# Kernel optimization log

Measured on AMD Instinct MI355X. Metric: run time of the kernel, lower is better.

The kernel has to match this reference:

```python
import jax, jax.numpy as jnp
import numpy as np

EMB = 128
HEADS = 8
B = 8
T = 2048


def setup_inputs() -> dict:
    key = jax.random.key(0)
    ks = jax.random.split(key, 6)
    x = jax.random.normal(ks[0], (B, T, EMB), dtype=jnp.float32)
    # torch Linear(emb, heads*emb, bias=False): store as (in, out) so y = x @ W
    scale = 1.0 / np.sqrt(EMB)
    Wq = jax.random.uniform(ks[1], (EMB, HEADS * EMB), jnp.float32, -scale, scale)
    Wk = jax.random.uniform(ks[2], (EMB, HEADS * EMB), jnp.float32, -scale, scale)
    Wv = jax.random.uniform(ks[3], (EMB, HEADS * EMB), jnp.float32, -scale, scale)
    so = 1.0 / np.sqrt(HEADS * EMB)
    Wo = jax.random.uniform(ks[4], (HEADS * EMB, EMB), jnp.float32, -so, so)
    bo = jax.random.uniform(ks[5], (EMB,), jnp.float32, -so, so)
    return {"x": x, "Wq": Wq, "Wk": Wk, "Wv": Wv, "Wo": Wo, "bo": bo}


def reference(x, Wq, Wk, Wv, Wo, bo):
    b, t, e = x.shape
    h = HEADS
    q = (x @ Wq).reshape(b, t, h, e)  # [b,t,h,e]
    k = (x @ Wk).reshape(b, t, h, e)
    v = (x @ Wv).reshape(b, t, h, e)
    # scores: [b,h,q,k], scaled by sqrt(e) (per-head dim == emb here)
    scores = jnp.einsum('bqhe,bkhe->bhqk', q, k) / jnp.sqrt(jnp.asarray(e, x.dtype))
    attn = jax.nn.softmax(scores, axis=-1)
    out = jnp.einsum('bhqk,bkhe->bqhe', attn, v).reshape(b, t, h * e)
    return out @ Wo + bo
```

## Files before the change

### kernel.cpp

```cpp
#include <hip/hip_runtime.h>

using bf16x8 = __attribute__((ext_vector_type(8))) short;
using f32x4  = __attribute__((ext_vector_type(4))) float;

__device__ __forceinline__ ushort f2bf(float f) {
    union { float f; unsigned int u; } c; c.f = f;
    unsigned int u = c.u;
    u = (u + 0x7fffu + ((u >> 16) & 1u)) >> 16;
    return (ushort)u;
}

#if defined(__has_builtin)
#if __has_builtin(__builtin_amdgcn_cvt_pk_bf16_f32)
#define HAS_PK_BF16 1
#endif
#endif
__device__ __forceinline__ unsigned int pkbf(float a, float b) {
#ifdef HAS_PK_BF16
    typedef __bf16 bf2 __attribute__((ext_vector_type(2)));
    union { bf2 v; unsigned int u; } cv;
    cv.v = __builtin_amdgcn_cvt_pk_bf16_f32(a, b);
    return cv.u;
#else
    return (unsigned int)f2bf(a) | ((unsigned int)f2bf(b) << 16);
#endif
}

__device__ __forceinline__ void dma16(const ushort* g, ushort* l) {
    __builtin_amdgcn_global_load_lds(
        (const __attribute__((address_space(1))) unsigned int*)g,
        (__attribute__((address_space(3))) unsigned int*)l, 16, 0, 0);
}

constexpr int BB   = 8;
constexpr int HH   = 8;
constexpr int TT   = 2048;
constexpr int DD   = 128;
#define C2F (0.08838834764831845f * 1.4426950408889634f)

__global__ void prep_kernel(const float* __restrict__ x,
                            const float* __restrict__ Wq, const float* __restrict__ Wk,
                            const float* __restrict__ Wv, const float* __restrict__ Wo,
                            ushort* __restrict__ xb, ushort* __restrict__ WqkvT,
                            ushort* __restrict__ WoT) {
    int t = blockIdx.x * 256 + threadIdx.x;
    if (t < 524288) {
        float4 v = ((const float4*)x)[t];
        ushort4 o;
        o.x = f2bf(v.x); o.y = f2bf(v.y); o.z = f2bf(v.z); o.w = f2bf(v.w);
        ((ushort4*)xb)[t] = o;
    } else if (t < 524288 + 393216) {
        int i = t - 524288;
        int j = i >> 7, kk = i & 127;
        const float* W = (j < 1024) ? Wq : ((j < 2048) ? Wk : Wv);
        int jj = j & 1023;
        WqkvT[j * 128 + kk] = f2bf(W[kk * 1024 + jj]);
    } else {
        int i = t - 917504;
        int e = i >> 10, kk = i & 1023;
        WoT[e * 1024 + kk] = f2bf(Wo[kk * 128 + e]);
    }
}

__global__ __launch_bounds__(256, 2)
void qkv_gemm(const ushort* __restrict__ xb, const ushort* __restrict__ WqkvT,
              ushort* __restrict__ q, ushort* __restrict__ k, ushort* __restrict__ vt) {
    __shared__ ushort Al[128 * 136];
    __shared__ ushort Bl[128 * 136];
    const int tid = threadIdx.x;
    const int n0 = blockIdx.x * 128, m0 = blockIdx.y * 128;

    for (int s = tid; s < 2048; s += 256) {
        int row = s >> 4, oct = s & 15;
        *(uint4*)&Al[row * 136 + oct * 8] = *(const uint4*)&xb[m0 * 128 + s * 8];
        *(uint4*)&Bl[row * 136 + oct * 8] = *(const uint4*)&WqkvT[n0 * 128 + s * 8];
    }
    __syncthreads();

    const int w = tid >> 6, lane = tid & 63, l15 = lane & 15, g = lane >> 4;
    const int wm = (w & 1) * 64, wn = (w >> 1) * 64;
    f32x4 acc[4][4] = {};

#pragma unroll
    for (int ks = 0; ks < 4; ks++) {
        bf16x8 af[4], bfr[4];
#pragma unroll
        for (int mb = 0; mb < 4; mb++)
            af[mb] = *(const bf16x8*)&Al[(wm + mb * 16 + l15) * 136 + ks * 32 + g * 8];
#pragma unroll
        for (int nb = 0; nb < 4; nb++)
            bfr[nb] = *(const bf16x8*)&Bl[(wn + nb * 16 + l15) * 136 + ks * 32 + g * 8];
#pragma unroll
        for (int mb = 0; mb < 4; mb++)
#pragma unroll
            for (int nb = 0; nb < 4; nb++)
                acc[mb][nb] = __builtin_amdgcn_mfma_f32_16x16x32_bf16(af[mb], bfr[nb], acc[mb][nb], 0, 0, 0);
    }

    const int which = n0 >> 10;
    const int b = m0 >> 11;
    const int h = (n0 >> 7) & 7;
    const int bh = b * HH + h;
    if (which == 0) {
#pragma unroll
        for (int mb = 0; mb < 4; mb++)
#pragma unroll
            for (int nb = 0; nb < 4; nb++)
#pragma unroll
                for (int r = 0; r < 4; r++) {
                    int t = (m0 + wm + mb * 16 + g * 4 + r) & 2047;
                    int e = wn + nb * 16 + l15;
                    q[((size_t)bh * TT + t) * DD + e] = f2bf(acc[mb][nb][r]);
                }
    } else if (which == 1) {
#pragma unroll
        for (int mb = 0; mb < 4; mb++)
#pragma unroll
            for (int nb = 0; nb < 4; nb++)
#pragma unroll
                for (int r = 0; r < 4; r++) {
                    int t = (m0 + wm + mb * 16 + g * 4 + r) & 2047;
                    int e = wn + nb * 16 + l15;
                    int esw = ((((e >> 3) ^ (t & 7)) << 3) | (e & 7));
                    k[((size_t)bh * TT + t) * DD + esw] = f2bf(acc[mb][nb][r]);
                }
    } else {
        __syncthreads();
        ushort* Tl = Al;
#pragma unroll
        for (int mb = 0; mb < 4; mb++)
#pragma unroll
            for (int nb = 0; nb < 4; nb++)
#pragma unroll
                for (int r = 0; r < 4; r++)
                    Tl[(wn + nb * 16 + l15) * 136 + wm + mb * 16 + g * 4 + r] = f2bf(acc[mb][nb][r]);
        __syncthreads();
        const int c0 = (m0 & 2047) >> 5;
        for (int s = tid; s < 2048; s += 256) {
            int e = s >> 4, x = s & 15;
            int cl = x >> 2, pos = x & 3;
            int el = e & 15;
            int vsw = (el ^ (el >> 2)) & 3;
            int tsrc = cl * 32 + ((pos ^ vsw) * 8);
            uint4 val = *(const uint4*)&Tl[e * 136 + tsrc];
            *(uint4*)&vt[(size_t)(((bh * 64 + c0 + cl) * 128) + e) * 32 + pos * 8] = val;
        }
    }
}

__global__ __launch_bounds__(256, 2)
void attn_kernel(const ushort* __restrict__ q, const ushort* __restrict__ k,
                 const ushort* __restrict__ vt, ushort* __restrict__ ao) {
    __shared__ ushort Kl[2][32 * 128];
    __shared__ ushort Vl[2][128 * 32];
    __shared__ ushort Pl[4 * 64 * 32];

    const int idx = blockIdx.x;
    const int qt256 = idx & 7, h = (idx >> 3) & 7, b = idx >> 6;
    const int t0 = qt256 * 256;
    const int bh = b * HH + h;
    const ushort* qg  = q  + (size_t)bh * TT * DD;
    const ushort* kg  = k  + (size_t)bh * TT * DD;
    const ushort* vtg = vt + (size_t)bh * 64 * DD * 32;

    const int tid = threadIdx.x, w = tid >> 6, lane = tid & 63;
    const int l15 = lane & 15, g = lane >> 4;
    const int swk = l15 & 7;
    const int swv = (l15 ^ (l15 >> 2)) & 3;

    bf16x8 qf[4][4];
#pragma unroll
    for (int qt = 0; qt < 4; qt++)
#pragma unroll
        for (int ks = 0; ks < 4; ks++)
            qf[qt][ks] = *(const bf16x8*)&qg[(size_t)(t0 + w * 64 + qt * 16 + l15) * DD + ks * 32 + g * 8];

    const int seg = tid * 8;
#pragma unroll
    for (int j = 0; j < 2; j++) {
        dma16(kg  + seg + j * 2048, &Kl[0][seg + j * 2048]);
        dma16(vtg + seg + j * 2048, &Vl[0][seg + j * 2048]);
    }

    f32x4 o[4][8] = {};
    float ls[4] = {0.0f, 0.0f, 0.0f, 0.0f};

    for (int c = 0; c < 64; c++) {
        const int cur = c & 1;
        __syncthreads();

        if (c < 63) {
            const ushort* kn = kg  + (size_t)(c + 1) * 4096;
            const ushort* vn = vtg + (size_t)(c + 1) * 4096;
#pragma unroll
            for (int j = 0; j < 2; j++) {
                dma16(kn + seg + j * 2048, &Kl[cur ^ 1][seg + j * 2048]);
                dma16(vn + seg + j * 2048, &Vl[cur ^ 1][seg + j * 2048]);
            }
        }

#pragma unroll
        for (int kt = 0; kt < 2; kt++) {
            f32x4 st[4] = {};
#pragma unroll
            for (int ks = 0; ks < 4; ks++) {
                bf16x8 kf = *(const bf16x8*)&Kl[cur][(kt * 16 + l15) * 128 + (((ks * 4 + g) ^ swk) * 8)];
#pragma unroll
                for (int qt = 0; qt < 4; qt++)
                    st[qt] = __builtin_amdgcn_mfma_f32_16x16x32_bf16(kf, qf[qt][ks], st[qt], 0, 0, 0);
            }
            const int kb = 2 * kt + (g >> 1);
#pragma unroll
            for (int qt = 0; qt < 4; qt++) {
                float p0 = __builtin_amdgcn_exp2f(st[qt][0] * C2F);
                float p1 = __builtin_amdgcn_exp2f(st[qt][1] * C2F);
                float p2 = __builtin_amdgcn_exp2f(st[qt][2] * C2F);
                float p3 = __builtin_amdgcn_exp2f(st[qt][3] * C2F);
                ls[qt] += (p0 + p1) + (p2 + p3);
                uint2 pk;
                pk.x = pkbf(p0, p1);
                pk.y = pkbf(p2, p3);
                *(uint2*)&Pl[w * 2048 + (qt * 16 + l15) * 32 + ((kb ^ swv) * 8) + (g & 1) * 4] = pk;
            }
        }

        {
            bf16x8 pa[4];
#pragma unroll
            for (int qt = 0; qt < 4; qt++)
                pa[qt] = *(const bf16x8*)&Pl[w * 2048 + (qt * 16 + l15) * 32 + ((g ^ swv) * 8)];
#pragma unroll
            for (int eb = 0; eb < 8; eb++) {
                bf16x8 vb = *(const bf16x8*)&Vl[cur][(eb * 16 + l15) * 32 + ((g ^ swv) * 8)];
#pragma unroll
                for (int qt = 0; qt < 4; qt++)
                    o[qt][eb] = __builtin_amdgcn_mfma_f32_16x16x32_bf16(pa[qt], vb, o[qt][eb], 0, 0, 0);
            }
        }
    }

#pragma unroll
    for (int qt = 0; qt < 4; qt++) {
        float tot = ls[qt];
        tot += __shfl_xor(tot, 16);
        tot += __shfl_xor(tot, 32);
        float inv[4];
#pragma unroll
        for (int r = 0; r < 4; r++)
            inv[r] = 1.0f / __shfl(tot, g * 4 + r, 64);
#pragma unroll
        for (int eb = 0; eb < 8; eb++)
#pragma unroll
            for (int r = 0; r < 4; r++) {
                int m = t0 + w * 64 + qt * 16 + g * 4 + r;
                int col = h * 128 + eb * 16 + l15;
                ao[(size_t)(b * TT + m) * 1024 + col] = f2bf(o[qt][eb][r] * inv[r]);
            }
    }
}

__global__ __launch_bounds__(256, 2)
void outproj_gemm(const ushort* __restrict__ ao, const ushort* __restrict__ WoT,
                  const float* __restrict__ bo, float* __restrict__ out) {
    __shared__ ushort Al[64 * 72];
    __shared__ ushort Bl[64 * 72];
    const int tid = threadIdx.x;
    const int n0 = blockIdx.x * 64, m0 = blockIdx.y * 64;
    const int w = tid >> 6, lane = tid & 63, l15 = lane & 15, g = lane >> 4;
    const int wm = (w & 1) * 32, wn = (w >> 1) * 32;
    f32x4 acc[2][2] = {};

    for (int kc = 0; kc < 16; kc++) {
        int k0 = kc * 64;
        __syncthreads();
        for (int s = tid; s < 512; s += 256) {
            int row = s >> 3, oct = s & 7;
            *(uint4*)&Al[row * 72 + oct * 8] = *(const uint4*)&ao[(size_t)(m0 + row) * 1024 + k0 + oct * 8];
            *(uint4*)&Bl[row * 72 + oct * 8] = *(const uint4*)&WoT[(n0 + row) * 1024 + k0 + oct * 8];
        }
        __syncthreads();
#pragma unroll
        for (int ks = 0; ks < 2; ks++) {
            bf16x8 af[2], bfr[2];
#pragma unroll
            for (int mb = 0; mb < 2; mb++)
                af[mb] = *(const bf16x8*)&Al[(wm + mb * 16 + l15) * 72 + ks * 32 + g * 8];
#pragma unroll
            for (int nb = 0; nb < 2; nb++)
                bfr[nb] = *(const bf16x8*)&Bl[(wn + nb * 16 + l15) * 72 + ks * 32 + g * 8];
#pragma unroll
            for (int mb = 0; mb < 2; mb++)
#pragma unroll
                for (int nb = 0; nb < 2; nb++)
                    acc[mb][nb] = __builtin_amdgcn_mfma_f32_16x16x32_bf16(af[mb], bfr[nb], acc[mb][nb], 0, 0, 0);
        }
    }

#pragma unroll
    for (int mb = 0; mb < 2; mb++)
#pragma unroll
        for (int nb = 0; nb < 2; nb++) {
            int j = n0 + wn + nb * 16 + l15;
            float bias = bo[j];
#pragma unroll
            for (int r = 0; r < 4; r++) {
                int m = m0 + wm + mb * 16 + g * 4 + r;
                out[(size_t)m * 128 + j] = acc[mb][nb][r] + bias;
            }
        }
}

extern "C" void kernel_launch(void* const* d_in, const int* in_sizes, int n_in,
                              void* d_out, int out_size, void* d_ws, size_t ws_size,
                              hipStream_t stream) {
    const float* x  = (const float*)d_in[0];
    const float* Wq = (const float*)d_in[1];
    const float* Wk = (const float*)d_in[2];
    const float* Wv = (const float*)d_in[3];
    const float* Wo = (const float*)d_in[4];
    const float* bo = (const float*)d_in[5];
    float* out = (float*)d_out;

    char* ws = (char*)d_ws;
    ushort* xb    = (ushort*)(ws);
    ushort* WqkvT = (ushort*)(ws + 4194304);
    ushort* WoT   = (ushort*)(ws + 4980736);
    ushort* qb    = (ushort*)(ws + 5242880);
    ushort* kb    = (ushort*)(ws + 38797312);
    ushort* vtb   = (ushort*)(ws + 72351744);
    ushort* ao    = (ushort*)(ws + 105906176);

    prep_kernel<<<4096, 256, 0, stream>>>(x, Wq, Wk, Wv, Wo, xb, WqkvT, WoT);
    qkv_gemm<<<dim3(24, 128), 256, 0, stream>>>(xb, WqkvT, qb, kb, vtb);
    attn_kernel<<<512, 256, 0, stream>>>(qb, kb, vtb, ao);
    outproj_gemm<<<dim3(2, 256), 256, 0, stream>>>(ao, WoT, bo, out);
}
```

Measured before the change: 275.0 us.

## Stage Q/K stores through LDS, fold softmax scale into Q, halve attention query tile

The QKV GEMM epilogue now writes Q and K tiles into shared memory first and then emits coalesced 16-byte global stores, where it used to do scattered 2-byte stores. The softmax scale constant is folded into Q at projection time, which removes a multiply per score in the attention loop. The attention kernel processes 128 queries per block instead of 256, with 1024 blocks, fewer accumulator registers and launch bounds raised to 3 blocks per CU, to improve occupancy and CU balance. The trade-off is that each K/V tile is loaded twice as many times overall, and folding the scale before the bf16 rounding of Q changes rounding slightly.

Measured after the change: 306.7 us. 1.12x slower.

```diff
diff --git a/kernel.cpp b/kernel.cpp
--- a/kernel.cpp
+++ b/kernel.cpp
@@ -101,32 +101,36 @@
     const int b = m0 >> 11;
     const int h = (n0 >> 7) & 7;
     const int bh = b * HH + h;
-    if (which == 0) {
+    const int tb = m0 & 2047;
+    __syncthreads();
+    ushort* Tl = Al;
+
+    if (which < 2) {
+        const float sc = (which == 0) ? C2F : 1.0f;
 #pragma unroll
         for (int mb = 0; mb < 4; mb++)
 #pragma unroll
             for (int nb = 0; nb < 4; nb++)
 #pragma unroll
-                for (int r = 0; r < 4; r++) {
-                    int t = (m0 + wm + mb * 16 + g * 4 + r) & 2047;
-                    int e = wn + nb * 16 + l15;
-                    q[((size_t)bh * TT + t) * DD + e] = f2bf(acc[mb][nb][r]);
-                }
-    } else if (which == 1) {
-#pragma unroll
-        for (int mb = 0; mb < 4; mb++)
-#pragma unroll
-            for (int nb = 0; nb < 4; nb++)
-#pragma unroll
-                for (int r = 0; r < 4; r++) {
-                    int t = (m0 + wm + mb * 16 + g * 4 + r) & 2047;
-                    int e = wn + nb * 16 + l15;
-                    int esw = ((((e >> 3) ^ (t & 7)) << 3) | (e & 7));
-                    k[((size_t)bh * TT + t) * DD + esw] = f2bf(acc[mb][nb][r]);
-                }
+                for (int r = 0; r < 4; r++)
+                    Tl[(wm + mb * 16 + g * 4 + r) * 136 + wn + nb * 16 + l15] =
+                        f2bf(acc[mb][nb][r] * sc);
+        __syncthreads();
+        ushort* dst = (which == 0) ? q : k;
+        if (which == 0) {
+            for (int s = tid; s < 2048; s += 256) {
+                int tl = s >> 4, oct = s & 15;
+                *(uint4*)&dst[((size_t)bh * TT + tb + tl) * DD + oct * 8] =
+                    *(const uint4*)&Tl[tl * 136 + oct * 8];
+            }
+        } else {
+            for (int s = tid; s < 2048; s += 256) {
+                int tl = s >> 4, oct = s & 15;
+                *(uint4*)&dst[((size_t)bh * TT + tb + tl) * DD + oct * 8] =
+                    *(const uint4*)&Tl[tl * 136 + ((oct ^ (tl & 7)) * 8)];
+            }
+        }
     } else {
-        __syncthreads();
-        ushort* Tl = Al;
 #pragma unroll
         for (int mb = 0; mb < 4; mb++)
 #pragma unroll
@@ -135,7 +139,7 @@
                 for (int r = 0; r < 4; r++)
                     Tl[(wn + nb * 16 + l15) * 136 + wm + mb * 16 + g * 4 + r] = f2bf(acc[mb][nb][r]);
         __syncthreads();
-        const int c0 = (m0 & 2047) >> 5;
+        const int c0 = tb >> 5;
         for (int s = tid; s < 2048; s += 256) {
             int e = s >> 4, x = s & 15;
             int cl = x >> 2, pos = x & 3;
@@ -148,16 +152,16 @@
     }
 }
 
-__global__ __launch_bounds__(256, 2)
+__global__ __launch_bounds__(256, 3)
 void attn_kernel(const ushort* __restrict__ q, const ushort* __restrict__ k,
                  const ushort* __restrict__ vt, ushort* __restrict__ ao) {
     __shared__ ushort Kl[2][32 * 128];
     __shared__ ushort Vl[2][128 * 32];
-    __shared__ ushort Pl[4 * 64 * 32];
+    __shared__ ushort Pl[4 * 32 * 32];
 
     const int idx = blockIdx.x;
-    const int qt256 = idx & 7, h = (idx >> 3) & 7, b = idx >> 6;
-    const int t0 = qt256 * 256;
+    const int qt128 = idx & 15, h = (idx >> 4) & 7, b = idx >> 7;
+    const int t0 = qt128 * 128;
     const int bh = b * HH + h;
     const ushort* qg  = q  + (size_t)bh * TT * DD;
     const ushort* kg  = k  + (size_t)bh * TT * DD;
@@ -168,12 +172,12 @@
     const int swk = l15 & 7;
     const int swv = (l15 ^ (l15 >> 2)) & 3;
 
-    bf16x8 qf[4][4];
-#pragma unroll
-    for (int qt = 0; qt < 4; qt++)
+    bf16x8 qf[2][4];
+#pragma unroll
+    for (int qt = 0; qt < 2; qt++)
 #pragma unroll
         for (int ks = 0; ks < 4; ks++)
-            qf[qt][ks] = *(const bf16x8*)&qg[(size_t)(t0 + w * 64 + qt * 16 + l15) * DD + ks * 32 + g * 8];
+            qf[qt][ks] = *(const bf16x8*)&qg[(size_t)(t0 + w * 32 + qt * 16 + l15) * DD + ks * 32 + g * 8];
 
     const int seg = tid * 8;
 #pragma unroll
@@ -182,8 +186,8 @@
         dma16(vtg + seg + j * 2048, &Vl[0][seg + j * 2048]);
     }
 
-    f32x4 o[4][8] = {};
-    float ls[4] = {0.0f, 0.0f, 0.0f, 0.0f};
+    f32x4 o[2][8] = {};
+    float ls[2] = {0.0f, 0.0f};
 
     for (int c = 0; c < 64; c++) {
         const int cur = c & 1;
@@ -201,46 +205,46 @@
 
 #pragma unroll
         for (int kt = 0; kt < 2; kt++) {
-            f32x4 st[4] = {};
+            f32x4 st[2] = {};
 #pragma unroll
             for (int ks = 0; ks < 4; ks++) {
                 bf16x8 kf = *(const bf16x8*)&Kl[cur][(kt * 16 + l15) * 128 + (((ks * 4 + g) ^ swk) * 8)];
 #pragma unroll
-                for (int qt = 0; qt < 4; qt++)
+                for (int qt = 0; qt < 2; qt++)
                     st[qt] = __builtin_amdgcn_mfma_f32_16x16x32_bf16(kf, qf[qt][ks], st[qt], 0, 0, 0);
             }
             const int kb = 2 * kt + (g >> 1);
 #pragma unroll
-            for (int qt = 0; qt < 4; qt++) {
-                float p0 = __builtin_amdgcn_exp2f(st[qt][0] * C2F);
-                float p1 = __builtin_amdgcn_exp2f(st[qt][1] * C2F);
-                float p2 = __builtin_amdgcn_exp2f(st[qt][2] * C2F);
-                float p3 = __builtin_amdgcn_exp2f(st[qt][3] * C2F);
+            for (int qt = 0; qt < 2; qt++) {
+                float p0 = __builtin_amdgcn_exp2f(st[qt][0]);
+                float p1 = __builtin_amdgcn_exp2f(st[qt][1]);
+                float p2 = __builtin_amdgcn_exp2f(st[qt][2]);
+                float p3 = __builtin_amdgcn_exp2f(st[qt][3]);
                 ls[qt] += (p0 + p1) + (p2 + p3);
                 uint2 pk;
                 pk.x = pkbf(p0, p1);
                 pk.y = pkbf(p2, p3);
-                *(uint2*)&Pl[w * 2048 + (qt * 16 + l15) * 32 + ((kb ^ swv) * 8) + (g & 1) * 4] = pk;
+                *(uint2*)&Pl[w * 1024 + (qt * 16 + l15) * 32 + ((kb ^ swv) * 8) + (g & 1) * 4] = pk;
             }
         }
 
         {
-            bf16x8 pa[4];
-#pragma unroll
-            for (int qt = 0; qt < 4; qt++)
-                pa[qt] = *(const bf16x8*)&Pl[w * 2048 + (qt * 16 + l15) * 32 + ((g ^ swv) * 8)];
+            bf16x8 pa[2];
+#pragma unroll
+            for (int qt = 0; qt < 2; qt++)
+                pa[qt] = *(const bf16x8*)&Pl[w * 1024 + (qt * 16 + l15) * 32 + ((g ^ swv) * 8)];
 #pragma unroll
             for (int eb = 0; eb < 8; eb++) {
                 bf16x8 vb = *(const bf16x8*)&Vl[cur][(eb * 16 + l15) * 32 + ((g ^ swv) * 8)];
 #pragma unroll
-                for (int qt = 0; qt < 4; qt++)
+                for (int qt = 0; qt < 2; qt++)
                     o[qt][eb] = __builtin_amdgcn_mfma_f32_16x16x32_bf16(pa[qt], vb, o[qt][eb], 0, 0, 0);
             }
         }
     }
 
 #pragma unroll
-    for (int qt = 0; qt < 4; qt++) {
+    for (int qt = 0; qt < 2; qt++) {
         float tot = ls[qt];
         tot += __shfl_xor(tot, 16);
         tot += __shfl_xor(tot, 32);
@@ -252,7 +256,7 @@
         for (int eb = 0; eb < 8; eb++)
 #pragma unroll
             for (int r = 0; r < 4; r++) {
-                int m = t0 + w * 64 + qt * 16 + g * 4 + r;
+                int m = t0 + w * 32 + qt * 16 + g * 4 + r;
                 int col = h * 128 + eb * 16 + l15;
                 ao[(size_t)(b * TT + m) * 1024 + col] = f2bf(o[qt][eb][r] * inv[r]);
             }
@@ -276,7 +280,7 @@
         for (int s = tid; s < 512; s += 256) {
             int row = s >> 3, oct = s & 7;
             *(uint4*)&Al[row * 72 + oct * 8] = *(const uint4*)&ao[(size_t)(m0 + row) * 1024 + k0 + oct * 8];
-            *(uint4*)&Bl[row * 72 + oct * 8] = *(const uint4*)&WoT[(n0 + row) * 1024 + k0 + oct * 8];
+            *(uint4*)&Bl[row * 72 + oct * 8] = *(const uint4*)&WoT[(size_t)(n0 + row) * 1024 + k0 + oct * 8];
         }
         __syncthreads();
 #pragma unroll
@@ -332,6 +336,6 @@
 
     prep_kernel<<<4096, 256, 0, stream>>>(x, Wq, Wk, Wv, Wo, xb, WqkvT, WoT);
     qkv_gemm<<<dim3(24, 128), 256, 0, stream>>>(xb, WqkvT, qb, kb, vtb);
-    attn_kernel<<<512, 256, 0, stream>>>(qb, kb, vtb, ao);
+    attn_kernel<<<1024, 256, 0, stream>>>(qb, kb, vtb, ao);
     outproj_gemm<<<dim3(2, 256), 256, 0, stream>>>(ao, WoT, bo, out);
 }
```

## Keep softmax probabilities in registers and pre-scale Q in projection

Applied to the files above, without the earlier changes.

The attention kernel no longer writes P to shared memory and reads it back. The exp2 outputs are packed straight into bf16x4 fragments and fed to 16x16x16 MFMAs, using a score layout that matches the A-operand layout. To make this work, the QKV GEMM swaps its MFMA operands so the accumulators are transposed, writes q/k as vectorized ushort4 stores, and folds the softmax scale C2F into Q. This removes LDS traffic and a round-trip per tile, but uses half-K MFMAs, which issue twice as many instructions for the PV product.

After: 308.3 us. +12.1%, slower.

```diff
diff --git a/kernel.cpp b/kernel.cpp
--- a/kernel.cpp
+++ b/kernel.cpp
@@ -1,7 +1,20 @@
 #include <hip/hip_runtime.h>
 
 using bf16x8 = __attribute__((ext_vector_type(8))) short;
+using bf16x4 = __attribute__((ext_vector_type(4))) short;
 using f32x4  = __attribute__((ext_vector_type(4))) float;
+
+#if defined(__HIP_DEVICE_COMPILE__)
+#if __has_builtin(__builtin_amdgcn_mfma_f32_16x16x16bf16_1k)
+#define MFMA16(a, b, c) __builtin_amdgcn_mfma_f32_16x16x16bf16_1k(a, b, c, 0, 0, 0)
+#elif __has_builtin(__builtin_amdgcn_mfma_f32_16x16x16_bf16)
+#define MFMA16(a, b, c) __builtin_amdgcn_mfma_f32_16x16x16_bf16(a, b, c, 0, 0, 0)
+#else
+#error "no 16x16x16 bf16 mfma builtin on device"
+#endif
+#else
+#define MFMA16(a, b, c) (c)
+#endif
 
 __device__ __forceinline__ ushort f2bf(float f) {
     union { float f; unsigned int u; } c; c.f = f;
@@ -10,13 +23,8 @@
     return (ushort)u;
 }
 
-#if defined(__has_builtin)
-#if __has_builtin(__builtin_amdgcn_cvt_pk_bf16_f32)
-#define HAS_PK_BF16 1
-#endif
-#endif
 __device__ __forceinline__ unsigned int pkbf(float a, float b) {
-#ifdef HAS_PK_BF16
+#if defined(__HIP_DEVICE_COMPILE__) && __has_builtin(__builtin_amdgcn_cvt_pk_bf16_f32)
     typedef __bf16 bf2 __attribute__((ext_vector_type(2)));
     union { bf2 v; unsigned int u; } cv;
     cv.v = __builtin_amdgcn_cvt_pk_bf16_f32(a, b);
@@ -79,52 +87,59 @@
 
     const int w = tid >> 6, lane = tid & 63, l15 = lane & 15, g = lane >> 4;
     const int wm = (w & 1) * 64, wn = (w >> 1) * 64;
-    f32x4 acc[4][4] = {};
-
-#pragma unroll
-    for (int ks = 0; ks < 4; ks++) {
-        bf16x8 af[4], bfr[4];
-#pragma unroll
-        for (int mb = 0; mb < 4; mb++)
-            af[mb] = *(const bf16x8*)&Al[(wm + mb * 16 + l15) * 136 + ks * 32 + g * 8];
-#pragma unroll
-        for (int nb = 0; nb < 4; nb++)
-            bfr[nb] = *(const bf16x8*)&Bl[(wn + nb * 16 + l15) * 136 + ks * 32 + g * 8];
-#pragma unroll
-        for (int mb = 0; mb < 4; mb++)
-#pragma unroll
-            for (int nb = 0; nb < 4; nb++)
-                acc[mb][nb] = __builtin_amdgcn_mfma_f32_16x16x32_bf16(af[mb], bfr[nb], acc[mb][nb], 0, 0, 0);
-    }
-
     const int which = n0 >> 10;
     const int b = m0 >> 11;
     const int h = (n0 >> 7) & 7;
     const int bh = b * HH + h;
-    if (which == 0) {
+    const int tb = m0 & 2047;
+    f32x4 acc[4][4] = {};
+
+    if (which < 2) {
+#pragma unroll
+        for (int ks = 0; ks < 4; ks++) {
+            bf16x8 af[4], bfr[4];
+#pragma unroll
+            for (int mb = 0; mb < 4; mb++)
+                af[mb] = *(const bf16x8*)&Al[(wm + mb * 16 + l15) * 136 + ks * 32 + g * 8];
+#pragma unroll
+            for (int nb = 0; nb < 4; nb++)
+                bfr[nb] = *(const bf16x8*)&Bl[(wn + nb * 16 + l15) * 136 + ks * 32 + g * 8];
+#pragma unroll
+            for (int mb = 0; mb < 4; mb++)
+#pragma unroll
+                for (int nb = 0; nb < 4; nb++)
+                    acc[mb][nb] = __builtin_amdgcn_mfma_f32_16x16x32_bf16(bfr[nb], af[mb], acc[mb][nb], 0, 0, 0);
+        }
+        const float sc = (which == 0) ? C2F : 1.0f;
+        ushort* dst = (which == 0) ? q : k;
 #pragma unroll
         for (int mb = 0; mb < 4; mb++)
 #pragma unroll
+            for (int nb = 0; nb < 4; nb++) {
+                int t = tb + wm + mb * 16 + l15;
+                int e0 = wn + nb * 16 + g * 4;
+                union { ushort4 v; ushort a[4]; } p4;
+#pragma unroll
+                for (int r = 0; r < 4; r++) p4.a[r] = f2bf(acc[mb][nb][r] * sc);
+                int ead = (which == 0) ? e0 : ((((e0 >> 3) ^ (t & 7)) << 3) | (e0 & 7));
+                *(ushort4*)&dst[((size_t)bh * TT + t) * DD + ead] = p4.v;
+            }
+    } else {
+#pragma unroll
+        for (int ks = 0; ks < 4; ks++) {
+            bf16x8 af[4], bfr[4];
+#pragma unroll
+            for (int mb = 0; mb < 4; mb++)
+                af[mb] = *(const bf16x8*)&Al[(wm + mb * 16 + l15) * 136 + ks * 32 + g * 8];
+#pragma unroll
             for (int nb = 0; nb < 4; nb++)
-#pragma unroll
-                for (int r = 0; r < 4; r++) {
-                    int t = (m0 + wm + mb * 16 + g * 4 + r) & 2047;
-                    int e = wn + nb * 16 + l15;
-                    q[((size_t)bh * TT + t) * DD + e] = f2bf(acc[mb][nb][r]);
-                }
-    } else if (which == 1) {
-#pragma unroll
-        for (int mb = 0; mb < 4; mb++)
-#pragma unroll
-            for (int nb = 0; nb < 4; nb++)
-#pragma unroll
-                for (int r = 0; r < 4; r++) {
-                    int t = (m0 + wm + mb * 16 + g * 4 + r) & 2047;
-                    int e = wn + nb * 16 + l15;
-                    int esw = ((((e >> 3) ^ (t & 7)) << 3) | (e & 7));
-                    k[((size_t)bh * TT + t) * DD + esw] = f2bf(acc[mb][nb][r]);
-                }
-    } else {
+                bfr[nb] = *(const bf16x8*)&Bl[(wn + nb * 16 + l15) * 136 + ks * 32 + g * 8];
+#pragma unroll
+            for (int mb = 0; mb < 4; mb++)
+#pragma unroll
+                for (int nb = 0; nb < 4; nb++)
+                    acc[mb][nb] = __builtin_amdgcn_mfma_f32_16x16x32_bf16(af[mb], bfr[nb], acc[mb][nb], 0, 0, 0);
+        }
         __syncthreads();
         ushort* Tl = Al;
 #pragma unroll
@@ -135,7 +150,7 @@
                 for (int r = 0; r < 4; r++)
                     Tl[(wn + nb * 16 + l15) * 136 + wm + mb * 16 + g * 4 + r] = f2bf(acc[mb][nb][r]);
         __syncthreads();
-        const int c0 = (m0 & 2047) >> 5;
+        const int c0 = tb >> 5;
         for (int s = tid; s < 2048; s += 256) {
             int e = s >> 4, x = s & 15;
             int cl = x >> 2, pos = x & 3;
@@ -153,7 +168,6 @@
                  const ushort* __restrict__ vt, ushort* __restrict__ ao) {
     __shared__ ushort Kl[2][32 * 128];
     __shared__ ushort Vl[2][128 * 32];
-    __shared__ ushort Pl[4 * 64 * 32];
 
     const int idx = blockIdx.x;
     const int qt256 = idx & 7, h = (idx >> 3) & 7, b = idx >> 6;
@@ -209,32 +223,26 @@
                 for (int qt = 0; qt < 4; qt++)
                     st[qt] = __builtin_amdgcn_mfma_f32_16x16x32_bf16(kf, qf[qt][ks], st[qt], 0, 0, 0);
             }
-            const int kb = 2 * kt + (g >> 1);
+            bf16x4 pa[4];
 #pragma unroll
             for (int qt = 0; qt < 4; qt++) {
-                float p0 = __builtin_amdgcn_exp2f(st[qt][0] * C2F);
-                float p1 = __builtin_amdgcn_exp2f(st[qt][1] * C2F);
-                float p2 = __builtin_amdgcn_exp2f(st[qt][2] * C2F);
-                float p3 = __builtin_amdgcn_exp2f(st[qt][3] * C2F);
+                float p0 = __builtin_amdgcn_exp2f(st[qt][0]);
+                float p1 = __builtin_amdgcn_exp2f(st[qt][1]);
+                float p2 = __builtin_amdgcn_exp2f(st[qt][2]);
+                float p3 = __builtin_amdgcn_exp2f(st[qt][3]);
                 ls[qt] += (p0 + p1) + (p2 + p3);
-                uint2 pk;
-                pk.x = pkbf(p0, p1);
-                pk.y = pkbf(p2, p3);
-                *(uint2*)&Pl[w * 2048 + (qt * 16 + l15) * 32 + ((kb ^ swv) * 8) + (g & 1) * 4] = pk;
-            }
-        }
-
-        {
-            bf16x8 pa[4];
-#pragma unroll
-            for (int qt = 0; qt < 4; qt++)
-                pa[qt] = *(const bf16x8*)&Pl[w * 2048 + (qt * 16 + l15) * 32 + ((g ^ swv) * 8)];
+                union { uint2 u; bf16x4 v; } pk;
+                pk.u.x = pkbf(p0, p1);
+                pk.u.y = pkbf(p2, p3);
+                pa[qt] = pk.v;
+            }
 #pragma unroll
             for (int eb = 0; eb < 8; eb++) {
-                bf16x8 vb = *(const bf16x8*)&Vl[cur][(eb * 16 + l15) * 32 + ((g ^ swv) * 8)];
+                bf16x4 vb = *(const bf16x4*)&Vl[cur][(eb * 16 + l15) * 32 +
+                                (((kt * 2 + (g >> 1)) ^ swv) * 8) + (g & 1) * 4];
 #pragma unroll
                 for (int qt = 0; qt < 4; qt++)
-                    o[qt][eb] = __builtin_amdgcn_mfma_f32_16x16x32_bf16(pa[qt], vb, o[qt][eb], 0, 0, 0);
+                    o[qt][eb] = MFMA16(pa[qt], vb, o[qt][eb]);
             }
         }
     }
@@ -276,7 +284,7 @@
         for (int s = tid; s < 512; s += 256) {
             int row = s >> 3, oct = s & 7;
             *(uint4*)&Al[row * 72 + oct * 8] = *(const uint4*)&ao[(size_t)(m0 + row) * 1024 + k0 + oct * 8];
-            *(uint4*)&Bl[row * 72 + oct * 8] = *(const uint4*)&WoT[(n0 + row) * 1024 + k0 + oct * 8];
+            *(uint4*)&Bl[row * 72 + oct * 8] = *(const uint4*)&WoT[(size_t)(n0 + row) * 1024 + k0 + oct * 8];
         }
         __syncthreads();
 #pragma unroll
```
